# Optimization experiments

Measured on AMD Instinct MI355X. Metric: run time of the kernel, lower is better.

Reference implementation:

```python
import jax, jax.numpy as jnp
import numpy as np

N_NODES = 100000
N_EDGES = 3200000
FEAT = 256
HIDDEN = 32
EMBED = 16


def gcn_conv(x, row, col, ew, W, b, num_nodes):
    """PyG GCNConv (add_self_loops=True, normalize=True) in eval mode.
    x: [N, Fin], row/col: [E] (source, target), ew: [E], W: [Fout, Fin], b: [Fout].
    """
    # add self loops with weight 1 (fill_value=1.0)
    loop = jnp.arange(num_nodes, dtype=row.dtype)
    row_f = jnp.concatenate([row, loop])
    col_f = jnp.concatenate([col, loop])
    ew_f = jnp.concatenate([ew, jnp.ones((num_nodes,), dtype=ew.dtype)])
    # symmetric normalization: deg over target (col) for source_to_target flow
    deg = jax.ops.segment_sum(ew_f, col_f, num_segments=num_nodes)
    dis = jnp.where(deg > 0, jax.lax.rsqrt(deg), 0.0)  # deg^{-1/2}, inf -> 0
    norm = dis[row_f] * ew_f * dis[col_f]  # [E+N]
    h = x @ W.T  # [N, Fout] -- linear (no bias) before propagate
    msg = h[row_f] * norm[:, None]  # gather + weight messages
    out = jax.ops.segment_sum(msg, col_f, num_segments=num_nodes)  # scatter-add
    return out + b


def setup_inputs() -> dict:
    key = jax.random.key(0)
    ks = jax.random.split(key, 8)
    x = jax.random.normal(ks[0], (N_NODES, FEAT), dtype=jnp.float32)
    ei = jax.random.randint(ks[1], (2, N_EDGES), 0, N_NODES, dtype=jnp.int64)
    ew = jax.random.uniform(ks[2], (N_EDGES,), dtype=jnp.float32)
    s1 = 1.0 / np.sqrt(FEAT)
    s2 = 1.0 / np.sqrt(HIDDEN)
    W1 = jax.random.uniform(ks[3], (HIDDEN, FEAT), minval=-s1, maxval=s1, dtype=jnp.float32)
    b1 = jax.random.uniform(ks[4], (HIDDEN,), minval=-s1, maxval=s1, dtype=jnp.float32)
    W2 = jax.random.uniform(ks[5], (EMBED, HIDDEN), minval=-s2, maxval=s2, dtype=jnp.float32)
    b2 = jax.random.uniform(ks[6], (EMBED,), minval=-s2, maxval=s2, dtype=jnp.float32)
    return {"x": x, "ei": ei, "ew": ew, "W1": W1, "b1": b1, "W2": W2, "b2": b2}


def reference(x, ei, ew, W1, b1, W2, b2):
    row, col = ei[0], ei[1]
    h = gcn_conv(x, row, col, ew, W1, b1, N_NODES)
    h = jax.nn.relu(h)
    # Dropout(0.25) and DropEdge(0.8) are identity in eval mode
    return gcn_conv(h, row, col, ew, W2, b2, N_NODES)
```

## Files before the change

kernel.cpp:

```cpp
#include <hip/hip_runtime.h>
#include <hip/hip_bf16.h>

#define N_NODES 100000
#define N_EDGES 3200000
#define FEAT 256
#define HIDDEN 32
#define EMBED 16
#define NPB 128
#define NBIN ((N_NODES + NPB - 1) / NPB)
#define CAPB 4608
#define OCAP 8192
#define GR 128
#define GS 68
#define G1N 32
#define G1CAP 2048
#define G2N 64
#define G2CAP 3072
#define PEPB 3072
#define PBLK ((N_EDGES + PEPB - 1) / PEPB)
#define OMS 784
#define RPT 5
#define NSK (NPB * 8)

__global__ void k_zero(int* __restrict__ ocur) {
    if (threadIdx.x == 0 && blockIdx.x == 0) *ocur = 0;
}

__global__ __launch_bounds__(256, 4) void k_part(
        const int* __restrict__ row, const int* __restrict__ col,
        const float* __restrict__ ew, int* __restrict__ offm,
        int2* __restrict__ chunks) {
    __shared__ int2 sed[PEPB];
    __shared__ int shist[NBIN];
    __shared__ int scur[NBIN];
    const int tid = threadIdx.x;
    const int blk = blockIdx.x;
    const int e0 = blk * PEPB;
    const int ne = min(PEPB, N_EDGES - e0);

    for (int i = tid; i < NBIN; i += 256) shist[i] = 0;
    __syncthreads();
    for (int i = tid; i < ne; i += 256) atomicAdd(&shist[col[e0 + i] >> 7], 1);
    __syncthreads();
    int l[4];
    int s = 0;
#pragma unroll
    for (int k = 0; k < 4; ++k) {
        int b = tid * 4 + k;
        l[k] = (b < NBIN) ? shist[b] : 0;
        s += l[k];
    }
    scur[tid] = s;
    __syncthreads();
    for (int d = 1; d < 256; d <<= 1) {
        int t = (tid >= d) ? scur[tid - d] : 0;
        __syncthreads();
        scur[tid] += t;
        __syncthreads();
    }
    int ex = scur[tid] - s;
    __syncthreads();
#pragma unroll
    for (int k = 0; k < 4; ++k) {
        int b = tid * 4 + k;
        if (b < NBIN) {
            shist[b] = ex;
            scur[b] = ex;
            ex += l[k];
        }
    }
    __syncthreads();
    for (int b = tid; b < NBIN; b += 256) offm[blk * OMS + b] = shist[b];
    if (tid == 0) offm[blk * OMS + NBIN] = ne;
    for (int i = tid; i < ne; i += 256) {
        int e = e0 + i;
        int c = col[e];
        int b = c >> 7;
        int p = atomicAdd(&scur[b], 1);
        sed[p] = make_int2(((c & (NPB - 1)) << 17) | row[e], __float_as_int(ew[e]));
    }
    __syncthreads();
    for (int i = tid; i < ne; i += 256) chunks[(size_t)blk * PEPB + i] = sed[i];
}

__global__ __launch_bounds__(256) void k_build(
        const int* __restrict__ offm, const int2* __restrict__ chunks,
        int2* __restrict__ binned, float* __restrict__ deg,
        int2* __restrict__ off2, int* __restrict__ binTot,
        int* __restrict__ ocur, int4* __restrict__ olist) {
    __shared__ int2 se[CAPB];
    __shared__ int scnt[NSK], scur2[NSK];
    __shared__ float sdeg[NPB];
    __shared__ int spart[256];
    const int bin = blockIdx.x, tid = threadIdx.x;
    const size_t base = (size_t)bin * CAPB;

    for (int i = tid; i < NSK; i += 256) scnt[i] = 0;
    for (int i = tid; i < NPB; i += 256) sdeg[i] = 0.f;
    int st[RPT], ln[RPT];
    int s = 0;
#pragma unroll
    for (int r = 0; r < RPT; ++r) {
        int k = tid * RPT + r;
        int a = 0, b2 = 0;
        if (k < PBLK) {
            a = offm[k * OMS + bin];
            b2 = offm[k * OMS + bin + 1];
        }
        st[r] = a;
        ln[r] = b2 - a;
        s += ln[r];
    }
    spart[tid] = s;
    __syncthreads();
    for (int d = 1; d < 256; d <<= 1) {
        int t = (tid >= d) ? spart[tid - d] : 0;
        __syncthreads();
        spart[tid] += t;
        __syncthreads();
    }
    int ex = spart[tid] - s;
    const int nTot = spart[255];
    const int n = min(nTot, CAPB);
    int dp = ex;
#pragma unroll
    for (int r = 0; r < RPT; ++r) {
        int k = tid * RPT + r;
        if (k < PBLK) {
            const int2* src = chunks + (size_t)k * PEPB + st[r];
            for (int j = 0; j < ln[r]; ++j) {
                int2 v = src[j];
                int lc = v.x >> 17;
                int dst = dp + j;
                if (dst < CAPB) {
                    se[dst] = v;
                    atomicAdd(&scnt[lc * 8 + ((v.x & 0x1FFFF) >> 14)], 1);
                    atomicAdd(&sdeg[lc], __int_as_float(v.y));
                } else {
                    int q = atomicAdd(ocur, 1);
                    if (q < OCAP)
                        olist[q] = make_int4(v.x & 0x1FFFF, bin * NPB + lc, v.y, 0);
                }
            }
            dp += ln[r];
        }
    }
    __syncthreads();
    int l0 = scnt[tid * 4], l1 = scnt[tid * 4 + 1],
        l2 = scnt[tid * 4 + 2], l3 = scnt[tid * 4 + 3];
    int s2 = l0 + l1 + l2 + l3;
    spart[tid] = s2;
    __syncthreads();
    for (int d = 1; d < 256; d <<= 1) {
        int t = (tid >= d) ? spart[tid - d] : 0;
        __syncthreads();
        spart[tid] += t;
        __syncthreads();
    }
    int ex2 = spart[tid] - s2;
    scnt[tid * 4] = ex2;
    scnt[tid * 4 + 1] = ex2 + l0;
    scnt[tid * 4 + 2] = ex2 + l0 + l1;
    scnt[tid * 4 + 3] = ex2 + l0 + l1 + l2;
    __syncthreads();
    for (int i = tid; i < NSK; i += 256) scur2[i] = scnt[i];
    __syncthreads();
    if (tid < NPB) {
        int node = bin * NPB + tid;
        if (node < N_NODES) {
            int stn = scnt[tid * 8];
            int en = (tid == NPB - 1) ? n : scnt[(tid + 1) * 8];
            off2[node] = make_int2((int)base + stn, en - stn);
            deg[node] = sdeg[tid] + 1.0f;
        }
    }
    if (tid == 0) binTot[bin] = n;
    __syncthreads();
    for (int i = tid; i < n; i += 256) {
        int2 v = se[i];
        int lc = v.x >> 17, src2 = v.x & 0x1FFFF;
        int p = atomicAdd(&scur2[lc * 8 + (src2 >> 14)], 1);
        binned[base + p] = make_int2(src2, v.y);
    }
}

__global__ void k_degover(const int* __restrict__ ocur, const int4* __restrict__ olist,
                          float* __restrict__ deg) {
    int p = blockIdx.x * blockDim.x + threadIdx.x;
    int n = min(*ocur, OCAP);
    if (p < n) { int4 t = olist[p]; unsafeAtomicAdd(&deg[t.y], __int_as_float(t.z)); }
}

__global__ void k_dis(float* __restrict__ deg) {
    int i = blockIdx.x * blockDim.x + threadIdx.x;
    if (i < N_NODES) {
        float d = deg[i];
        deg[i] = (d > 0.0f) ? rsqrtf(d) : 0.0f;
    }
}

__global__ void k_wnorm(const int* __restrict__ binTot, int2* __restrict__ csr,
                        const float* __restrict__ dis) {
    int bin = blockIdx.x;
    int n = binTot[bin];
    size_t base = (size_t)bin * CAPB;
    for (int i = threadIdx.x; i < n; i += 256) {
        int2 v = csr[base + i];
        float w = __int_as_float(v.y) * dis[v.x];
        csr[base + i] = make_int2(v.x, __float_as_int(w));
    }
}

__global__ __launch_bounds__(256) void k_gemm1(
        const float* __restrict__ x, const float* __restrict__ W1,
        float* __restrict__ h) {
    __shared__ float sx[GR][GS];
    __shared__ float sw[HIDDEN][GS];

    const int tid = threadIdx.x;
    const size_t base = (size_t)blockIdx.x * GR;
    const float4* x4 = (const float4*)x;
    const float4* w4 = (const float4*)W1;

    const int r0 = tid >> 3;
    const int c0 = tid & 7;
    float acc[4][4] = {};

#pragma unroll
    for (int p = 0; p < 4; ++p) {
        for (int i = tid; i < GR * 16; i += 256) {
            int r = i >> 4, kq = i & 15;
            float4 v = make_float4(0.f, 0.f, 0.f, 0.f);
            if (base + r < N_NODES) v = x4[(base + r) * 64 + p * 16 + kq];
            *(float4*)&sx[r][kq * 4] = v;
        }
        for (int i = tid; i < HIDDEN * 16; i += 256) {
            int f = i >> 4, kq = i & 15;
            *(float4*)&sw[f][kq * 4] = w4[f * 64 + p * 16 + kq];
        }
        __syncthreads();

#pragma unroll 4
        for (int kq = 0; kq < 16; ++kq) {
            float4 xa[4], wv[4];
#pragma unroll
            for (int m = 0; m < 4; ++m) xa[m] = *(const float4*)&sx[r0 + 32 * m][kq * 4];
#pragma unroll
            for (int j = 0; j < 4; ++j) wv[j] = *(const float4*)&sw[c0 + 8 * j][kq * 4];
#pragma unroll
            for (int m = 0; m < 4; ++m)
#pragma unroll
                for (int j = 0; j < 4; ++j)
                    acc[m][j] += xa[m].x * wv[j].x + xa[m].y * wv[j].y +
                                 xa[m].z * wv[j].z + xa[m].w * wv[j].w;
        }
        __syncthreads();
    }

#pragma unroll
    for (int m = 0; m < 4; ++m) {
        size_t r = base + r0 + 32 * m;
        if (r < N_NODES) {
#pragma unroll
            for (int j = 0; j < 4; ++j) h[r * HIDDEN + c0 + 8 * j] = acc[m][j];
        }
    }
}

__global__ __launch_bounds__(256) void k_gather1(
        const int2* __restrict__ off2, const int2* __restrict__ csr,
        const float* __restrict__ h, const float* __restrict__ dis,
        const float* __restrict__ b1, float* __restrict__ out1) {
    __shared__ int2 sc[G1CAP];
    __shared__ int s_start, s_n;
    const int tid = threadIdx.x;
    const int node0 = blockIdx.x * G1N;
    if (tid == 0) {
        int2 a = off2[node0];
        int2 b = off2[node0 + G1N - 1];
        s_start = a.x;
        s_n = b.x + b.y - a.x;
    }
    __syncthreads();
    const int start = s_start, n = s_n;
    const bool fit = (n <= G1CAP);
    if (fit) for (int i = tid; i < n; i += 256) sc[i] = csr[start + i];
    __syncthreads();

    const int node = node0 + (tid >> 3);
    const int og = tid & 7;
    float d = dis[node];
    float d2 = d * d;
    float4 self = *(const float4*)(h + (size_t)node * HIDDEN + og * 4);
    float4 bv = *(const float4*)(b1 + og * 4);
    float4 acc = make_float4(0.f, 0.f, 0.f, 0.f);

    int2 o = off2[node];
    for (int j = 0; j < o.y; ++j) {
        int2 v = fit ? sc[o.x - start + j] : csr[o.x + j];
        float w = __int_as_float(v.y);
        const float4 hv = *(const float4*)(h + (size_t)v.x * HIDDEN + og * 4);
        acc.x += hv.x * w; acc.y += hv.y * w; acc.z += hv.z * w; acc.w += hv.w * w;
    }
    *(float4*)(out1 + (size_t)node * HIDDEN + og * 4) =
        make_float4(acc.x * d + self.x * d2 + bv.x, acc.y * d + self.y * d2 + bv.y,
                    acc.z * d + self.z * d2 + bv.z, acc.w * d + self.w * d2 + bv.w);
}

__global__ void k_over1(const int* __restrict__ ocur, const int4* __restrict__ olist,
                        const float* __restrict__ dis, const float* __restrict__ h,
                        float* __restrict__ out1) {
    int p = blockIdx.x * blockDim.x + threadIdx.x;
    int n = min(*ocur, OCAP);
    if (p < n) {
        int4 t = olist[p];
        int r = t.x, c = t.y;
        float w = dis[r] * __int_as_float(t.z) * dis[c];
        for (int f = 0; f < HIDDEN; ++f)
            unsafeAtomicAdd(&out1[(size_t)c * HIDDEN + f], h[(size_t)r * HIDDEN + f] * w);
    }
}

__global__ void k_gemm2(const float* __restrict__ out1, const float* __restrict__ W2,
                        float* __restrict__ h2) {
    int t = blockIdx.x * blockDim.x + threadIdx.x;
    int i = t >> 4;
    if (i >= N_NODES) return;
    int f = t & 15;
    const float* r = out1 + (size_t)i * HIDDEN;
    const float* w = W2 + f * HIDDEN;
    float acc = 0.f;
#pragma unroll
    for (int k = 0; k < HIDDEN; ++k) acc += fmaxf(r[k], 0.f) * w[k];
    h2[(size_t)i * EMBED + f] = acc;
}

__global__ __launch_bounds__(256) void k_gather2(
        const int2* __restrict__ off2, const int2* __restrict__ csr,
        const float* __restrict__ h2, const float* __restrict__ dis,
        const float* __restrict__ b2, float* __restrict__ out) {
    __shared__ int2 sc[G2CAP];
    __shared__ int s_start, s_n;
    const int tid = threadIdx.x;
    const int node0 = blockIdx.x * G2N;
    const int lastn = min(node0 + G2N, N_NODES) - 1;
    if (tid == 0) {
        int2 a = off2[node0];
        int2 b = off2[lastn];
        s_start = a.x;
        s_n = b.x + b.y - a.x;
    }
    __syncthreads();
    const int start = s_start, n = s_n;
    const bool fit = (n <= G2CAP);
    if (fit) for (int i = tid; i < n; i += 256) sc[i] = csr[start + i];
    __syncthreads();

    const int node = node0 + (tid >> 2);
    const int og = tid & 3;
    if (node >= N_NODES) return;
    float d = dis[node];
    float d2 = d * d;
    float4 self = *(const float4*)(h2 + (size_t)node * EMBED + og * 4);
    float4 bv = *(const float4*)(b2 + og * 4);
    float4 acc = make_float4(0.f, 0.f, 0.f, 0.f);

    int2 o = off2[node];
    for (int j = 0; j < o.y; ++j) {
        int2 v = fit ? sc[o.x - start + j] : csr[o.x + j];
        float w = __int_as_float(v.y);
        const float4 hv = *(const float4*)(h2 + (size_t)v.x * EMBED + og * 4);
        acc.x += hv.x * w; acc.y += hv.y * w; acc.z += hv.z * w; acc.w += hv.w * w;
    }
    *(float4*)(out + (size_t)node * EMBED + og * 4) =
        make_float4(acc.x * d + self.x * d2 + bv.x, acc.y * d + self.y * d2 + bv.y,
                    acc.z * d + self.z * d2 + bv.z, acc.w * d + self.w * d2 + bv.w);
}

__global__ void k_over2(const int* __restrict__ ocur, const int4* __restrict__ olist,
                        const float* __restrict__ dis, const float* __restrict__ h2,
                        float* __restrict__ out) {
    int p = blockIdx.x * blockDim.x + threadIdx.x;
    int n = min(*ocur, OCAP);
    if (p < n) {
        int4 t = olist[p];
        int r = t.x, c = t.y;
        float w = dis[r] * __int_as_float(t.z) * dis[c];
        for (int f = 0; f < EMBED; ++f)
            unsafeAtomicAdd(&out[(size_t)c * EMBED + f], h2[(size_t)r * EMBED + f] * w);
    }
}

extern "C" void kernel_launch(void* const* d_in, const int* in_sizes, int n_in,
                              void* d_out, int out_size, void* d_ws, size_t ws_size,
                              hipStream_t stream) {
    const float* x  = (const float*)d_in[0];
    const int*   ei = (const int*)d_in[1];
    const float* ew = (const float*)d_in[2];
    const float* W1 = (const float*)d_in[3];
    const float* b1 = (const float*)d_in[4];
    const float* W2 = (const float*)d_in[5];
    const float* b2 = (const float*)d_in[6];
    float* out = (float*)d_out;

    const int* row = ei;
    const int* col = ei + N_EDGES;

    int2*  off2   = (int2*)d_ws;
    int2*  binned = off2 + N_NODES;
    float* deg    = (float*)(binned + (size_t)NBIN * CAPB);
    int*   binTot = (int*)(deg + N_NODES);
    int*   offm   = binTot + 784;
    int*   ocur   = offm + (size_t)PBLK * OMS;
    int4*  olist  = (int4*)(ocur + 4);
    void*  big    = (void*)(olist + OCAP);
    int2*  chunks = (int2*)big;
    float* h      = (float*)big;
    float* out1   = h + (size_t)N_NODES * HIDDEN;
    float* h2     = h;

    const int B = 256;
    const int gN = (N_NODES + B - 1) / B;
    const int gO = (OCAP + B - 1) / B;

    k_zero<<<1, 64, 0, stream>>>(ocur);
    k_part<<<PBLK, B, 0, stream>>>(row, col, ew, offm, chunks);
    k_build<<<NBIN, B, 0, stream>>>(offm, chunks, binned, deg, off2, binTot, ocur, olist);
    k_degover<<<gO, B, 0, stream>>>(ocur, olist, deg);
    k_dis<<<gN, B, 0, stream>>>(deg);
    k_wnorm<<<NBIN, B, 0, stream>>>(binTot, binned, deg);
    k_gemm1<<<(N_NODES + GR - 1) / GR, B, 0, stream>>>(x, W1, h);
    k_gather1<<<N_NODES / G1N, B, 0, stream>>>(off2, binned, h, deg, b1, out1);
    k_over1<<<gO, B, 0, stream>>>(ocur, olist, deg, h, out1);
    k_gemm2<<<(N_NODES * 16 + B - 1) / B, B, 0, stream>>>(out1, W2, h2);
    k_gather2<<<(N_NODES + G2N - 1) / G2N, B, 0, stream>>>(off2, binned, h2, deg, b2, out);
    k_over2<<<gO, B, 0, stream>>>(ocur, olist, deg, h2, out);
}
```

Before: 320.0 us.

## Preload full W1 into shared memory and register-prefetch x tiles in gemm1

The first-layer GEMM now loads all of W1 into shared memory once instead of re-staging it each K-chunk. The x tile is split into 8 smaller 32-wide K slices, and the next slice is prefetched into registers while the current one is computed. This overlaps global loads of x with FMA work and cuts per-chunk W reloads. In exchange it uses more barriers per block, and the larger W buffer plus staging registers may change occupancy.

```diff
diff --git a/kernel.cpp b/kernel.cpp
--- a/kernel.cpp
+++ b/kernel.cpp
@@ -11,7 +11,6 @@
 #define CAPB 4608
 #define OCAP 8192
 #define GR 128
-#define GS 68
 #define G1N 32
 #define G1CAP 2048
 #define G2N 64
@@ -214,39 +213,51 @@
 __global__ __launch_bounds__(256) void k_gemm1(
         const float* __restrict__ x, const float* __restrict__ W1,
         float* __restrict__ h) {
-    __shared__ float sx[GR][GS];
-    __shared__ float sw[HIDDEN][GS];
+    __shared__ float sx[GR][36];
+    __shared__ float sw[HIDDEN][260];
 
     const int tid = threadIdx.x;
     const size_t base = (size_t)blockIdx.x * GR;
     const float4* x4 = (const float4*)x;
     const float4* w4 = (const float4*)W1;
+    const int rs = tid >> 3;
+    const int ks = tid & 7;
+
+    for (int i = tid; i < HIDDEN * 64; i += 256) {
+        int f = i >> 6, kq = i & 63;
+        *(float4*)&sw[f][kq * 4] = w4[f * 64 + kq];
+    }
+    float4 stg[4];
+#pragma unroll
+    for (int m = 0; m < 4; ++m) {
+        int rr = rs + 32 * m;
+        stg[m] = make_float4(0.f, 0.f, 0.f, 0.f);
+        if (base + rr < N_NODES) stg[m] = x4[(base + rr) * 64 + ks];
+    }
+#pragma unroll
+    for (int m = 0; m < 4; ++m) *(float4*)&sx[rs + 32 * m][ks * 4] = stg[m];
+    __syncthreads();
 
     const int r0 = tid >> 3;
     const int c0 = tid & 7;
     float acc[4][4] = {};
 
-#pragma unroll
-    for (int p = 0; p < 4; ++p) {
-        for (int i = tid; i < GR * 16; i += 256) {
-            int r = i >> 4, kq = i & 15;
-            float4 v = make_float4(0.f, 0.f, 0.f, 0.f);
-            if (base + r < N_NODES) v = x4[(base + r) * 64 + p * 16 + kq];
-            *(float4*)&sx[r][kq * 4] = v;
-        }
-        for (int i = tid; i < HIDDEN * 16; i += 256) {
-            int f = i >> 4, kq = i & 15;
-            *(float4*)&sw[f][kq * 4] = w4[f * 64 + p * 16 + kq];
-        }
-        __syncthreads();
-
-#pragma unroll 4
-        for (int kq = 0; kq < 16; ++kq) {
+    for (int p = 0; p < 8; ++p) {
+        if (p < 7) {
+#pragma unroll
+            for (int m = 0; m < 4; ++m) {
+                int rr = rs + 32 * m;
+                stg[m] = make_float4(0.f, 0.f, 0.f, 0.f);
+                if (base + rr < N_NODES) stg[m] = x4[(base + rr) * 64 + (p + 1) * 8 + ks];
+            }
+        }
+#pragma unroll
+        for (int kq = 0; kq < 8; ++kq) {
             float4 xa[4], wv[4];
 #pragma unroll
             for (int m = 0; m < 4; ++m) xa[m] = *(const float4*)&sx[r0 + 32 * m][kq * 4];
 #pragma unroll
-            for (int j = 0; j < 4; ++j) wv[j] = *(const float4*)&sw[c0 + 8 * j][kq * 4];
+            for (int j = 0; j < 4; ++j) wv[j] = *(const float4*)&sw[c0 + 8 * j][(p * 8 + kq) * 4];
 #pragma unroll
             for (int m = 0; m < 4; ++m)
 #pragma unroll
@@ -255,6 +266,11 @@
                                  xa[m].z * wv[j].z + xa[m].w * wv[j].w;
         }
         __syncthreads();
+        if (p < 7) {
+#pragma unroll
+            for (int m = 0; m < 4; ++m) *(float4*)&sx[rs + 32 * m][ks * 4] = stg[m];
+            __syncthreads();
+        }
     }
 
 #pragma unroll
```

Result: slower. 329.1 us (+2.9%).
